# Performance work log

Measured on AMD Instinct MI355X. Metric: run time of the kernel, lower is better.

The kernel has to match this reference:

```python
import jax, jax.numpy as jnp
import numpy as np

STRIDE = 1  # module init arg


def setup_inputs() -> dict:
    key = jax.random.key(0)
    k1, k2 = jax.random.split(key)
    x = jax.random.normal(k1, (16, 32, 256, 256), dtype=jnp.float32)
    kernel = jax.random.normal(k2, (32, 5, 5), dtype=jnp.float32) * 0.1
    return {"input": x, "kernel": kernel}


def _maxmin_conv(x, kernel, stride=STRIDE):
    # Max-min semifield convolution:
    #   out[b,oc,i,j] = max_{c,dy,dx} min(x_pad[b,c,i*s+dy,j*s+dx], k[oc,dy,dx])
    # Since min(., k) is monotone in x, the max over in-channels commutes:
    #   max_{c} min(x_c, k) == min(max_c x_c, k)
    # so we reduce channels once up front (same math, far less memory).
    K = kernel.shape[-1]
    p = K - 1
    top = p // 2
    bot = p - top  # calculate_padding(): left=top=floor(p/2), right=bottom=p-top
    xmax = jnp.max(x, axis=1)  # [B, H, W]
    xp = jnp.pad(xmax, ((0, 0), (top, bot), (top, bot)), constant_values=-np.inf)
    B, Hp, Wp = xp.shape
    Ho = (Hp - K) // stride + 1
    Wo = (Wp - K) // stride + 1
    OC = kernel.shape[0]
    acc = jnp.full((B, OC, Ho, Wo), -np.inf, dtype=x.dtype)
    for dy in range(K):  # fixed small K*K loop over kernel taps
        for dx in range(K):
            patch = xp[:, dy:dy + stride * Ho:stride, dx:dx + stride * Wo:stride]  # [B,Ho,Wo]
            cand = jnp.minimum(patch[:, None, :, :], kernel[None, :, dy, dx, None, None])
            acc = jnp.maximum(acc, cand)
    return acc


def reference(input, kernel):
    return _maxmin_conv(input, kernel)
```

## Files before the change

### kernel.cpp

```cpp
#include <hip/hip_runtime.h>
#include <math.h>


#define BATCH 16
#define CH    32
#define OCH   32
#define HH    256
#define WW    256
#define HWSZ  (HH * WW)
#define TW    32
#define TH    16
#define LH    20
#define LW    42
#define NWG   (BATCH * (HH / TH) * (WW / TW))

typedef float floatx4 __attribute__((ext_vector_type(4)));

__device__ __forceinline__ float vmax3(float a, float b, float c) {
    float d;
    asm("v_max3_f32 %0, %1, %2, %3" : "=v"(d) : "v"(a), "v"(b), "v"(c));
    return d;
}

__global__ __launch_bounds__(256, 2) void fused_maxmin_kernel(const float* __restrict__ x,
                                                              const float* __restrict__ kk,
                                                              float* __restrict__ out) {
    __shared__ float xmt[LH][LW];
    int tid = threadIdx.x;
    int bid = blockIdx.x;
    int swz = (bid & 7) * (NWG >> 3) + (bid >> 3);
    int b   = swz >> 7;
    int t2  = swz & 127;
    int ty  = t2 >> 3;
    int tx  = t2 & 7;

    const float NI = -INFINITY;

    if (tid < 200) {
        int pr = tid / 10;
        int pc = tid % 10;
        int c4 = tx * 8 - 1 + pc;
        int rw = ty * TH - 2 + pr;
        bool valid = (c4 >= 0) && (c4 < WW / 4) && (rw >= 0) && (rw < HH);
        int c4c = c4 < 0 ? 0 : (c4 > WW / 4 - 1 ? WW / 4 - 1 : c4);
        int rwc = rw < 0 ? 0 : (rw > HH - 1 ? HH - 1 : rw);
        const float4* src = (const float4*)x + (size_t)b * CH * (HWSZ / 4)
                          + (size_t)rwc * (WW / 4) + c4c;
        float4 m = src[0];
#pragma unroll
        for (int c = 1; c < CH; ++c) {
            float4 v = src[(size_t)c * (HWSZ / 4)];
            m.x = fmaxf(m.x, v.x);
            m.y = fmaxf(m.y, v.y);
            m.z = fmaxf(m.z, v.z);
            m.w = fmaxf(m.w, v.w);
        }
        if (!valid) { m.x = NI; m.y = NI; m.z = NI; m.w = NI; }
        *(float2*)&xmt[pr][4 * pc]     = make_float2(m.x, m.y);
        *(float2*)&xmt[pr][4 * pc + 2] = make_float2(m.z, m.w);
    }
    __syncthreads();

    int xg = tid & 7;
    int rg = (tid >> 3) & 7;
    int wv = __builtin_amdgcn_readfirstlane(tid >> 6);

    float w[6][8];
#pragma unroll
    for (int r = 0; r < 6; ++r) {
        const float* rp = &xmt[2 * rg + r][4 * xg + 2];
#pragma unroll
        for (int s = 0; s < 4; ++s)
            *(float2*)&w[r][2 * s] = *(const float2*)(rp + 2 * s);
    }

    size_t obase = (size_t)(b * OCH + wv * 8) * HWSZ
                 + (size_t)(ty * TH + 2 * rg) * WW + tx * TW + 4 * xg;

    for (int o = 0; o < 8; ++o) {
        const float* kw = kk + (wv * 8 + o) * 25;
        float kr[25];
#pragma unroll
        for (int i = 0; i < 25; ++i) kr[i] = kw[i];

        float* op = out + obase + (size_t)o * HWSZ;
#pragma unroll
        for (int r = 0; r < 2; ++r) {
            float a[4];
#pragma unroll
            for (int j = 0; j < 4; ++j) {
                float m[25];
#pragma unroll
                for (int dy = 0; dy < 5; ++dy)
#pragma unroll
                    for (int dx = 0; dx < 5; ++dx)
                        m[dy * 5 + dx] = fminf(w[r + dy][j + dx], kr[dy * 5 + dx]);
                float t0 = vmax3(m[0],  m[1],  m[2]);
                float t1 = vmax3(m[3],  m[4],  m[5]);
                float t2 = vmax3(m[6],  m[7],  m[8]);
                float t3 = vmax3(m[9],  m[10], m[11]);
                float t4 = vmax3(m[12], m[13], m[14]);
                float t5 = vmax3(m[15], m[16], m[17]);
                float t6 = vmax3(m[18], m[19], m[20]);
                float t7 = vmax3(m[21], m[22], m[23]);
                float u0 = vmax3(t0, t1, t2);
                float u1 = vmax3(t3, t4, t5);
                float u2 = vmax3(t6, t7, m[24]);
                a[j] = vmax3(u0, u1, u2);
            }
            floatx4 ov = { a[0], a[1], a[2], a[3] };
            __builtin_nontemporal_store(ov, (floatx4*)(op + (size_t)r * WW));
        }
    }
}

extern "C" void kernel_launch(void* const* d_in, const int* in_sizes, int n_in,
                              void* d_out, int out_size, void* d_ws, size_t ws_size,
                              hipStream_t stream) {
    const float* x  = (const float*)d_in[0];
    const float* kk = (const float*)d_in[1];
    float* out      = (float*)d_out;
    fused_maxmin_kernel<<<NWG, 256, 0, stream>>>(x, kk, out);
}
```

Measured before the change: 55.40 us.

## Process two row tiles per workgroup, overlapping next tile's channel-max loads with compute

```diff
diff --git a/kernel.cpp b/kernel.cpp
--- a/kernel.cpp
+++ b/kernel.cpp
@@ -12,7 +12,7 @@
 #define TH    16
 #define LH    20
 #define LW    42
-#define NWG   (BATCH * (HH / TH) * (WW / TW))
+#define NWG   (BATCH * (HH / (2 * TH)) * (WW / TW))
 
 typedef float floatx4 __attribute__((ext_vector_type(4)));
 
@@ -22,42 +22,73 @@
     return d;
 }
 
+__device__ __forceinline__ void conv_oc(const float (&w)[6][8], const float* __restrict__ kk,
+                                        int oc, float* __restrict__ out, size_t obq) {
+    const float* kw = kk + oc * 25;
+    float kr[25];
+#pragma unroll
+    for (int i = 0; i < 25; ++i) kr[i] = kw[i];
+#pragma unroll
+    for (int r = 0; r < 2; ++r) {
+        float a[4];
+#pragma unroll
+        for (int j = 0; j < 4; ++j) {
+            float mm[25];
+#pragma unroll
+            for (int dy = 0; dy < 5; ++dy)
+#pragma unroll
+                for (int dx = 0; dx < 5; ++dx)
+                    mm[dy * 5 + dx] = fminf(w[r + dy][j + dx], kr[dy * 5 + dx]);
+            float t0 = vmax3(mm[0],  mm[1],  mm[2]);
+            float t1 = vmax3(mm[3],  mm[4],  mm[5]);
+            float t2 = vmax3(mm[6],  mm[7],  mm[8]);
+            float t3 = vmax3(mm[9],  mm[10], mm[11]);
+            float t4 = vmax3(mm[12], mm[13], mm[14]);
+            float t5 = vmax3(mm[15], mm[16], mm[17]);
+            float t6 = vmax3(mm[18], mm[19], mm[20]);
+            float t7 = vmax3(mm[21], mm[22], mm[23]);
+            a[j] = vmax3(vmax3(t0, t1, t2), vmax3(t3, t4, t5), vmax3(t6, t7, mm[24]));
+        }
+        floatx4 ov = { a[0], a[1], a[2], a[3] };
+        __builtin_nontemporal_store(ov, (floatx4*)(out + obq + (size_t)r * WW));
+    }
+}
+
 __global__ __launch_bounds__(256, 2) void fused_maxmin_kernel(const float* __restrict__ x,
                                                               const float* __restrict__ kk,
                                                               float* __restrict__ out) {
-    __shared__ float xmt[LH][LW];
+    __shared__ float xmt[2][LH][LW];
     int tid = threadIdx.x;
     int bid = blockIdx.x;
     int swz = (bid & 7) * (NWG >> 3) + (bid >> 3);
-    int b   = swz >> 7;
-    int t2  = swz & 127;
-    int ty  = t2 >> 3;
+    int b   = swz >> 6;
+    int t2  = swz & 63;
+    int ty2 = t2 >> 3;
     int tx  = t2 & 7;
 
     const float NI = -INFINITY;
 
+    int pr = tid / 10, pc = tid % 10;
+    int c4 = tx * 8 - 1 + pc;
+    bool cvalid = (c4 >= 0) && (c4 < WW / 4);
+    int c4c = c4 < 0 ? 0 : (c4 > WW / 4 - 1 ? WW / 4 - 1 : c4);
+    const float4* xb4 = (const float4*)x + (size_t)b * CH * (HWSZ / 4);
+
     if (tid < 200) {
-        int pr = tid / 10;
-        int pc = tid % 10;
-        int c4 = tx * 8 - 1 + pc;
-        int rw = ty * TH - 2 + pr;
-        bool valid = (c4 >= 0) && (c4 < WW / 4) && (rw >= 0) && (rw < HH);
-        int c4c = c4 < 0 ? 0 : (c4 > WW / 4 - 1 ? WW / 4 - 1 : c4);
+        int rw = ty2 * 32 - 2 + pr;
+        bool valid = cvalid && (rw >= 0) && (rw < HH);
         int rwc = rw < 0 ? 0 : (rw > HH - 1 ? HH - 1 : rw);
-        const float4* src = (const float4*)x + (size_t)b * CH * (HWSZ / 4)
-                          + (size_t)rwc * (WW / 4) + c4c;
+        const float4* src = xb4 + (size_t)rwc * (WW / 4) + c4c;
         float4 m = src[0];
 #pragma unroll
         for (int c = 1; c < CH; ++c) {
             float4 v = src[(size_t)c * (HWSZ / 4)];
-            m.x = fmaxf(m.x, v.x);
-            m.y = fmaxf(m.y, v.y);
-            m.z = fmaxf(m.z, v.z);
-            m.w = fmaxf(m.w, v.w);
+            m.x = fmaxf(m.x, v.x); m.y = fmaxf(m.y, v.y);
+            m.z = fmaxf(m.z, v.z); m.w = fmaxf(m.w, v.w);
         }
         if (!valid) { m.x = NI; m.y = NI; m.z = NI; m.w = NI; }
-        *(float2*)&xmt[pr][4 * pc]     = make_float2(m.x, m.y);
-        *(float2*)&xmt[pr][4 * pc + 2] = make_float2(m.z, m.w);
+        *(float2*)&xmt[0][pr][4 * pc]     = make_float2(m.x, m.y);
+        *(float2*)&xmt[0][pr][4 * pc + 2] = make_float2(m.z, m.w);
     }
     __syncthreads();
 
@@ -65,53 +96,60 @@
     int rg = (tid >> 3) & 7;
     int wv = __builtin_amdgcn_readfirstlane(tid >> 6);
 
+    int rw1 = ty2 * 32 + 14 + pr;
+    bool valid1 = cvalid && (rw1 < HH);
+    int rwc1 = rw1 > HH - 1 ? HH - 1 : rw1;
+    const float4* src1 = xb4 + (size_t)rwc1 * (WW / 4) + c4c;
+
     float w[6][8];
 #pragma unroll
     for (int r = 0; r < 6; ++r) {
-        const float* rp = &xmt[2 * rg + r][4 * xg + 2];
+        const float* rp = &xmt[0][2 * rg + r][4 * xg + 2];
 #pragma unroll
         for (int s = 0; s < 4; ++s)
             *(float2*)&w[r][2 * s] = *(const float2*)(rp + 2 * s);
     }
 
-    size_t obase = (size_t)(b * OCH + wv * 8) * HWSZ
-                 + (size_t)(ty * TH + 2 * rg) * WW + tx * TW + 4 * xg;
+    size_t ob0 = (size_t)(b * OCH + wv * 8) * HWSZ
+               + (size_t)(ty2 * 32 + 2 * rg) * WW + tx * TW + 4 * xg;
 
+    float4 macc = make_float4(NI, NI, NI, NI);
+    bool act = tid < 200;
+#pragma unroll
     for (int o = 0; o < 8; ++o) {
-        const float* kw = kk + (wv * 8 + o) * 25;
-        float kr[25];
-#pragma unroll
-        for (int i = 0; i < 25; ++i) kr[i] = kw[i];
-
-        float* op = out + obase + (size_t)o * HWSZ;
-#pragma unroll
-        for (int r = 0; r < 2; ++r) {
-            float a[4];
-#pragma unroll
-            for (int j = 0; j < 4; ++j) {
-                float m[25];
-#pragma unroll
-                for (int dy = 0; dy < 5; ++dy)
-#pragma unroll
-                    for (int dx = 0; dx < 5; ++dx)
-                        m[dy * 5 + dx] = fminf(w[r + dy][j + dx], kr[dy * 5 + dx]);
-                float t0 = vmax3(m[0],  m[1],  m[2]);
-                float t1 = vmax3(m[3],  m[4],  m[5]);
-                float t2 = vmax3(m[6],  m[7],  m[8]);
-                float t3 = vmax3(m[9],  m[10], m[11]);
-                float t4 = vmax3(m[12], m[13], m[14]);
-                float t5 = vmax3(m[15], m[16], m[17]);
-                float t6 = vmax3(m[18], m[19], m[20]);
-                float t7 = vmax3(m[21], m[22], m[23]);
-                float u0 = vmax3(t0, t1, t2);
-                float u1 = vmax3(t3, t4, t5);
-                float u2 = vmax3(t6, t7, m[24]);
-                a[j] = vmax3(u0, u1, u2);
-            }
-            floatx4 ov = { a[0], a[1], a[2], a[3] };
-            __builtin_nontemporal_store(ov, (floatx4*)(op + (size_t)r * WW));
+        float4 v0, v1, v2, v3;
+        if (act) {
+            v0 = src1[(size_t)(4 * o + 0) * (HWSZ / 4)];
+            v1 = src1[(size_t)(4 * o + 1) * (HWSZ / 4)];
+            v2 = src1[(size_t)(4 * o + 2) * (HWSZ / 4)];
+            v3 = src1[(size_t)(4 * o + 3) * (HWSZ / 4)];
+        }
+        conv_oc(w, kk, wv * 8 + o, out, ob0 + (size_t)o * HWSZ);
+        if (act) {
+            macc.x = fmaxf(macc.x, fmaxf(fmaxf(v0.x, v1.x), fmaxf(v2.x, v3.x)));
+            macc.y = fmaxf(macc.y, fmaxf(fmaxf(v0.y, v1.y), fmaxf(v2.y, v3.y)));
+            macc.z = fmaxf(macc.z, fmaxf(fmaxf(v0.z, v1.z), fmaxf(v2.z, v3.z)));
+            macc.w = fmaxf(macc.w, fmaxf(fmaxf(v0.w, v1.w), fmaxf(v2.w, v3.w)));
         }
     }
+    if (act) {
+        if (!valid1) { macc.x = NI; macc.y = NI; macc.z = NI; macc.w = NI; }
+        *(float2*)&xmt[1][pr][4 * pc]     = make_float2(macc.x, macc.y);
+        *(float2*)&xmt[1][pr][4 * pc + 2] = make_float2(macc.z, macc.w);
+    }
+    __syncthreads();
+
+#pragma unroll
+    for (int r = 0; r < 6; ++r) {
+        const float* rp = &xmt[1][2 * rg + r][4 * xg + 2];
+#pragma unroll
+        for (int s = 0; s < 4; ++s)
+            *(float2*)&w[r][2 * s] = *(const float2*)(rp + 2 * s);
+    }
+    size_t ob1 = ob0 + (size_t)16 * WW;
+#pragma unroll
+    for (int o = 0; o < 8; ++o)
+        conv_oc(w, kk, wv * 8 + o, out, ob1 + (size_t)o * HWSZ);
 }
 
 extern "C" void kernel_launch(void* const* d_in, const int* in_sizes, int n_in,
```

Result: slower. 58.43 us (+5.5%).

## Sort kernel taps descending and exit the tap loop early per wave

Applied to the files above, without the earlier changes.

```diff
diff --git a/kernel.cpp b/kernel.cpp
--- a/kernel.cpp
+++ b/kernel.cpp
@@ -16,16 +16,28 @@
 
 typedef float floatx4 __attribute__((ext_vector_type(4)));
 
-__device__ __forceinline__ float vmax3(float a, float b, float c) {
-    float d;
-    asm("v_max3_f32 %0, %1, %2, %3" : "=v"(d) : "v"(a), "v"(b), "v"(c));
-    return d;
+__global__ void sort_taps_kernel(const float* __restrict__ kk, float2* __restrict__ ent) {
+    int t = threadIdx.x;
+    if (t >= OCH * 25) return;
+    int oc = t / 25, i = t % 25;
+    float ki = kk[oc * 25 + i];
+    int rank = 0;
+#pragma unroll
+    for (int j = 0; j < 25; ++j) {
+        float kj = kk[oc * 25 + j];
+        rank += (kj > ki) || (kj == ki && j < i);
+    }
+    int dy = i / 5, dx = i % 5;
+    int off = 4 * (dy * LW + dx);
+    ent[oc * 26 + rank] = make_float2(ki, __int_as_float(off));
+    if (i == 0) ent[oc * 26 + 25] = make_float2(-INFINITY, __int_as_float(0));
 }
 
 __global__ __launch_bounds__(256, 2) void fused_maxmin_kernel(const float* __restrict__ x,
-                                                              const float* __restrict__ kk,
+                                                              const float2* __restrict__ gent,
                                                               float* __restrict__ out) {
     __shared__ float xmt[LH][LW];
+    __shared__ float2 ent[OCH * 26];
     int tid = threadIdx.x;
     int bid = blockIdx.x;
     int swz = (bid & 7) * (NWG >> 3) + (bid >> 3);
@@ -35,6 +47,8 @@
     int tx  = t2 & 7;
 
     const float NI = -INFINITY;
+
+    for (int i = tid; i < OCH * 26; i += 256) ent[i] = gent[i];
 
     if (tid < 200) {
         int pr = tid / 10;
@@ -65,52 +79,42 @@
     int rg = (tid >> 3) & 7;
     int wv = __builtin_amdgcn_readfirstlane(tid >> 6);
 
-    float w[6][8];
-#pragma unroll
-    for (int r = 0; r < 6; ++r) {
-        const float* rp = &xmt[2 * rg + r][4 * xg + 2];
-#pragma unroll
-        for (int s = 0; s < 4; ++s)
-            *(float2*)&w[r][2 * s] = *(const float2*)(rp + 2 * s);
-    }
+    const char* r0p = (const char*)&xmt[2 * rg][4 * xg + 2];
+    const char* r1p = (const char*)&xmt[2 * rg + 1][4 * xg + 2];
 
     size_t obase = (size_t)(b * OCH + wv * 8) * HWSZ
                  + (size_t)(ty * TH + 2 * rg) * WW + tx * TW + 4 * xg;
 
     for (int o = 0; o < 8; ++o) {
-        const float* kw = kk + (wv * 8 + o) * 25;
-        float kr[25];
-#pragma unroll
-        for (int i = 0; i < 25; ++i) kr[i] = kw[i];
+        const float2* E = &ent[(wv * 8 + o) * 26];
+        float a00 = NI, a01 = NI, a02 = NI, a03 = NI;
+        float a10 = NI, a11 = NI, a12 = NI, a13 = NI;
+
+        for (int i = 0; i < 25; ++i) {
+            float2 e  = E[i];
+            float  kn = E[i + 1].x;
+            float  kv = e.x;
+            int    off = __float_as_int(e.y);
+            const float* p0 = (const float*)(r0p + off);
+            const float* p1 = (const float*)(r1p + off);
+            a00 = fmaxf(a00, fminf(p0[0], kv));
+            a01 = fmaxf(a01, fminf(p0[1], kv));
+            a02 = fmaxf(a02, fminf(p0[2], kv));
+            a03 = fmaxf(a03, fminf(p0[3], kv));
+            a10 = fmaxf(a10, fminf(p1[0], kv));
+            a11 = fmaxf(a11, fminf(p1[1], kv));
+            a12 = fmaxf(a12, fminf(p1[2], kv));
+            a13 = fmaxf(a13, fminf(p1[3], kv));
+            float mn = fminf(fminf(fminf(a00, a01), fminf(a02, a03)),
+                             fminf(fminf(a10, a11), fminf(a12, a13)));
+            if (__all(mn >= kn)) break;
+        }
 
         float* op = out + obase + (size_t)o * HWSZ;
-#pragma unroll
-        for (int r = 0; r < 2; ++r) {
-            float a[4];
-#pragma unroll
-            for (int j = 0; j < 4; ++j) {
-                float m[25];
-#pragma unroll
-                for (int dy = 0; dy < 5; ++dy)
-#pragma unroll
-                    for (int dx = 0; dx < 5; ++dx)
-                        m[dy * 5 + dx] = fminf(w[r + dy][j + dx], kr[dy * 5 + dx]);
-                float t0 = vmax3(m[0],  m[1],  m[2]);
-                float t1 = vmax3(m[3],  m[4],  m[5]);
-                float t2 = vmax3(m[6],  m[7],  m[8]);
-                float t3 = vmax3(m[9],  m[10], m[11]);
-                float t4 = vmax3(m[12], m[13], m[14]);
-                float t5 = vmax3(m[15], m[16], m[17]);
-                float t6 = vmax3(m[18], m[19], m[20]);
-                float t7 = vmax3(m[21], m[22], m[23]);
-                float u0 = vmax3(t0, t1, t2);
-                float u1 = vmax3(t3, t4, t5);
-                float u2 = vmax3(t6, t7, m[24]);
-                a[j] = vmax3(u0, u1, u2);
-            }
-            floatx4 ov = { a[0], a[1], a[2], a[3] };
-            __builtin_nontemporal_store(ov, (floatx4*)(op + (size_t)r * WW));
-        }
+        floatx4 o0 = { a00, a01, a02, a03 };
+        floatx4 o1 = { a10, a11, a12, a13 };
+        __builtin_nontemporal_store(o0, (floatx4*)op);
+        __builtin_nontemporal_store(o1, (floatx4*)(op + WW));
     }
 }
 
@@ -120,5 +124,8 @@
     const float* x  = (const float*)d_in[0];
     const float* kk = (const float*)d_in[1];
     float* out      = (float*)d_out;
-    fused_maxmin_kernel<<<NWG, 256, 0, stream>>>(x, kk, out);
+    float2* ent     = (float2*)d_ws;
+
+    sort_taps_kernel<<<1, OCH * 25, 0, stream>>>(kk, ent);
+    fused_maxmin_kernel<<<NWG, 256, 0, stream>>>(x, ent, out);
 }
```

Result: no change. 54.55 us, median of 2 (-1.5%).
